# Performance work log

Hardware: AMD Instinct MI355X
Metric: run time of the kernel (lower is better)

Reference implementation:

```python
import jax, jax.numpy as jnp
import numpy as np

HEIGHT, WIDTH = 224, 224
SIGMA = 3e-4      # soft-coverage falloff (DIB-R style delta)
EPS = 1e-10


def setup_inputs() -> dict:
    key = jax.random.key(0)
    kp, kf, kc = jax.random.split(key, 3)
    B, P, F = 2, 2048, 256
    points = 0.5 * jax.random.normal(kp, (B, P, 3), dtype=jnp.float32)
    faces = jax.random.randint(kf, (F, 3), 0, P, dtype=jnp.int32)
    colors = jax.random.uniform(kc, (B, P, 3), dtype=jnp.float32)
    rot = jnp.broadcast_to(jnp.eye(3, dtype=jnp.float32), (B, 3, 3))
    pos = jnp.tile(jnp.array([0.0, 0.0, 2.5], jnp.float32), (B, 1))
    tanfov = float(np.tan(45.0 * np.pi / 360.0))
    proj = jnp.array([[1.0 / tanfov], [1.0 / tanfov], [-1.0]], jnp.float32)
    return dict(points_bxpx3=points, faces_fx3=faces, camera_rot=rot,
                camera_pos=pos, camera_proj=proj, colors_bxpx3=colors)


def _render(points_bxpx3, camera_rot, camera_pos, camera_proj, colors_bxpx3, faces_fx3):
    H, W = HEIGHT, WIDTH
    # ---- perspective projection (kaolin DIB-R convention) ----
    pc = jnp.einsum('bpj,bij->bpi', points_bxpx3 - camera_pos[:, None, :], camera_rot)  # camera space [B,P,3]
    xyz = pc * camera_proj.reshape(1, 1, 3)
    xy = xyz[..., :2] / xyz[..., 2:3]                                   # NDC xy [B,P,2]
    i0, i1, i2 = faces_fx3[:, 0], faces_fx3[:, 1], faces_fx3[:, 2]
    p0, p1, p2 = pc[:, i0], pc[:, i1], pc[:, i2]                        # [B,F,3]
    q0, q1, q2 = xy[:, i0], xy[:, i1], xy[:, i2]                        # [B,F,2]
    normal = jnp.cross(p1 - p0, p2 - p0)                                # [B,F,3]
    normalz = normal[..., 2]
    normal1 = normal / jnp.sqrt(jnp.sum(normal * normal, -1, keepdims=True) + EPS)
    # ---- per-face vertex features: 3 verts x (rgb + mask) == color_bxfx12 ----
    ones = jnp.ones(colors_bxpx3.shape[:2] + (1,), colors_bxpx3.dtype)
    cm = jnp.concatenate([colors_bxpx3, ones], -1)                      # [B,P,4]
    feat = jnp.stack([cm[:, i0], cm[:, i1], cm[:, i2]], axis=2)         # [B,F,3,4]
    # ---- rasterize: per-pixel per-face barycentric test ----
    xs = (2.0 * jnp.arange(W, dtype=jnp.float32) + 1.0) / W - 1.0
    ys = 1.0 - (2.0 * jnp.arange(H, dtype=jnp.float32) + 1.0) / H
    PX = xs[None, None, :, None]                                        # [1,1,W,1]
    PY = ys[None, :, None, None]                                        # [1,H,1,1]
    bf = lambda a: a[:, None, None, :]                                  # [B,F] -> [B,1,1,F]
    x0, y0 = q0[..., 0], q0[..., 1]
    x1, y1 = q1[..., 0], q1[..., 1]
    x2, y2 = q2[..., 0], q2[..., 1]
    denom = (y1 - y2) * (x0 - x2) + (x2 - x1) * (y0 - y2)
    denom = jnp.where(jnp.abs(denom) < EPS, EPS, denom)
    dx2 = PX - bf(x2)
    dy2 = PY - bf(y2)
    lam0 = (bf(y1 - y2) * dx2 + bf(x2 - x1) * dy2) / bf(denom)          # [B,H,W,F]
    lam1 = (bf(y2 - y0) * dx2 + bf(x0 - x2) * dy2) / bf(denom)
    lam2 = 1.0 - lam0 - lam1
    inside = (lam0 >= 0) & (lam1 >= 0) & (lam2 >= 0)
    front = (normalz > 0)[:, None, None, :]
    valid = inside & front
    # nearest face: camera looks down -z, nearer == larger camera-space z
    zpix = lam0 * bf(p0[..., 2]) + lam1 * bf(p1[..., 2]) + lam2 * bf(p2[..., 2])
    score = jnp.where(valid, zpix, -1e10)
    idx = jnp.argmax(score, axis=-1)                                    # [B,H,W]
    valid_any = jnp.any(valid, axis=-1)
    take = lambda a: jnp.take_along_axis(a, idx[..., None], axis=-1)[..., 0]
    l0, l1, l2 = take(lam0), take(lam1), take(lam2)
    fsel = jax.vmap(lambda f, i: f[i])(feat, idx)                       # [B,H,W,3,4]
    imfeat = (l0[..., None] * fsel[..., 0, :] + l1[..., None] * fsel[..., 1, :]
              + l2[..., None] * fsel[..., 2, :]) * valid_any[..., None]
    # ---- soft coverage probability: dist to nearest edge, 0 inside ----
    def seg_d2(ax, ay, bx, by):
        ex, ey = bf(bx - ax), bf(by - ay)
        pax, pay = PX - bf(ax), PY - bf(ay)
        t = jnp.clip((pax * ex + pay * ey) / (ex * ex + ey * ey + EPS), 0.0, 1.0)
        ddx, ddy = pax - t * ex, pay - t * ey
        return ddx * ddx + ddy * ddy
    d2 = jnp.minimum(seg_d2(x0, y0, x1, y1),
                     jnp.minimum(seg_d2(x1, y1, x2, y2), seg_d2(x2, y2, x0, y0)))
    d2 = jnp.where(inside, 0.0, d2)
    prob = jnp.where(front, jnp.exp(-d2 / SIGMA) * (1.0 - 1e-7), 0.0)
    improb = (1.0 - jnp.exp(jnp.sum(jnp.log1p(-prob), axis=-1)))[..., None]  # [B,H,W,1]
    imrender = imfeat[..., :3]
    return imrender, improb, normal1


def reference(points_bxpx3, camera_rot, camera_pos, camera_proj, colors_bxpx3, faces_fx3):
    return _render(points_bxpx3, camera_rot, camera_pos, camera_proj, colors_bxpx3, faces_fx3)
```

## Files before the change

kernel.cpp:

```cpp
#include <hip/hip_runtime.h>
#include <math.h>

#define HGT 224
#define WID 224
#define NPIX (HGT * WID)
#define SIGMA 0.0003f
#define EPSV 1e-10f
#define DATA_STRIDE 32
#define LDS_STRIDE 33
#define MAXF 256
#define MARGIN 0.062f
#define HALFDIAG 0.04420f
#define BAND (MARGIN + HALFDIAG)
#define HD_IN (HALFDIAG + 1.0e-4f)


__global__ void face_pre(const float* __restrict__ points,
                         const int* __restrict__ faces,
                         const float* __restrict__ rot,
                         const float* __restrict__ pos,
                         const float* __restrict__ proj,
                         const float* __restrict__ colors,
                         float* __restrict__ filt,
                         float* __restrict__ data,
                         float* __restrict__ out_normal,
                         int B, int P, int F) {
    int gid = blockIdx.x * blockDim.x + threadIdx.x;
    if (gid >= B * F) return;
    int b = gid / F;
    int f = gid - b * F;

    const float* Rb = rot + b * 9;
    float posx = pos[b * 3 + 0], posy = pos[b * 3 + 1], posz = pos[b * 3 + 2];
    float pj0 = proj[0], pj1 = proj[1], pj2 = proj[2];

    float pcx[3], pcy[3], pcz[3], qx[3], qy[3], col[9];
    for (int v = 0; v < 3; v++) {
        int i = faces[f * 3 + v];
        float dx = points[(b * P + i) * 3 + 0] - posx;
        float dy = points[(b * P + i) * 3 + 1] - posy;
        float dz = points[(b * P + i) * 3 + 2] - posz;
        pcx[v] = Rb[0] * dx + Rb[1] * dy + Rb[2] * dz;
        pcy[v] = Rb[3] * dx + Rb[4] * dy + Rb[5] * dz;
        pcz[v] = Rb[6] * dx + Rb[7] * dy + Rb[8] * dz;
        float zz = pcz[v] * pj2;
        qx[v] = (pcx[v] * pj0) / zz;
        qy[v] = (pcy[v] * pj1) / zz;
        col[v * 3 + 0] = colors[(b * P + i) * 3 + 0];
        col[v * 3 + 1] = colors[(b * P + i) * 3 + 1];
        col[v * 3 + 2] = colors[(b * P + i) * 3 + 2];
    }

    float ux = pcx[1] - pcx[0], uy = pcy[1] - pcy[0], uz = pcz[1] - pcz[0];
    float vx = pcx[2] - pcx[0], vy = pcy[2] - pcy[0], vz = pcz[2] - pcz[0];
    float nx = uy * vz - uz * vy;
    float ny = uz * vx - ux * vz;
    float nz = ux * vy - uy * vx;
    float ninv = 1.0f / sqrtf(nx * nx + ny * ny + nz * nz + EPSV);
    out_normal[gid * 3 + 0] = nx * ninv;
    out_normal[gid * 3 + 1] = ny * ninv;
    out_normal[gid * 3 + 2] = nz * ninv;

    float x0 = qx[0], y0 = qy[0], x1 = qx[1], y1 = qy[1], x2 = qx[2], y2 = qy[2];
    float denom = (y1 - y2) * (x0 - x2) + (x2 - x1) * (y0 - y2);
    if (fabsf(denom) < EPSV) denom = EPSV;
    float rd = 1.0f / denom;

    float a00 = (y1 - y2) * rd;
    float a01 = (x2 - x1) * rd;
    float a10 = (y2 - y0) * rd;
    float a11 = (x0 - x2) * rd;

    float z0 = pcz[0], z1 = pcz[1], z2c = pcz[2];
    float zgx = a00 * (z0 - z2c) + a10 * (z1 - z2c);
    float zgy = a01 * (z0 - z2c) + a11 * (z1 - z2c);
    float zc  = z2c - zgx * x2 - zgy * y2;

    int BF = B * F;
    float4* f4 = (float4*)filt;
    bool front = nz > 0.0f;
    if (front) {
        f4[0 * BF + gid] = make_float4(fminf(x0, fminf(x1, x2)),
                                       fminf(y0, fminf(y1, y2)),
                                       fmaxf(x0, fmaxf(x1, x2)),
                                       fmaxf(y0, fmaxf(y1, y2)));
    } else {
        f4[0 * BF + gid] = make_float4(1e30f, 1e30f, -1e30f, -1e30f);
    }

    float n0 = 1.0f / sqrtf(a00 * a00 + a01 * a01 + EPSV);
    float n1 = 1.0f / sqrtf(a10 * a10 + a11 * a11 + EPSV);
    float g2x = -(a00 + a10), g2y = -(a01 + a11);
    float n2 = 1.0f / sqrtf(g2x * g2x + g2y * g2y + EPSV);
    f4[1 * BF + gid] = make_float4(a00 * n0, a01 * n0,
                                   -(a00 * x2 + a01 * y2) * n0, a10 * n1);
    f4[2 * BF + gid] = make_float4(a11 * n1, -(a10 * x2 + a11 * y2) * n1,
                                   g2x * n2, g2y * n2);
    f4[3 * BF + gid] = make_float4((1.0f - g2x * x2 - g2y * y2) * n2,
                                   zgx, zgy, zc);

    float* fp = data + gid * DATA_STRIDE;
    fp[0] = x2; fp[1] = y2;
    fp[2] = zgx; fp[3] = zgy; fp[4] = z2c;
    fp[5] = a00; fp[6] = a01; fp[7] = a10; fp[8] = a11;
    fp[9] = x0; fp[10] = y0; fp[11] = x1; fp[12] = y1;

    float e01x = x1 - x0, e01y = y1 - y0;
    float e12x = x2 - x1, e12y = y2 - y1;
    float e20x = x0 - x2, e20y = y0 - y2;
    fp[13] = e01x; fp[14] = e01y; fp[15] = 1.0f / (e01x * e01x + e01y * e01y + EPSV);
    fp[16] = e12x; fp[17] = e12y; fp[18] = 1.0f / (e12x * e12x + e12y * e12y + EPSV);
    fp[19] = e20x; fp[20] = e20y; fp[21] = 1.0f / (e20x * e20x + e20y * e20y + EPSV);
    for (int k = 0; k < 9; k++) fp[22 + k] = col[k];
    fp[31] = 0.0f;
}

__device__ __forceinline__ float seg_d2(float px, float py, float ax, float ay,
                                        float ex, float ey, float inv) {
    float pax = px - ax, pay = py - ay;
    float t = (pax * ex + pay * ey) * inv;
    t = fminf(fmaxf(t, 0.0f), 1.0f);
    float ddx = pax - t * ex;
    float ddy = pay - t * ey;
    return ddx * ddx + ddy * ddy;
}

__global__ __launch_bounds__(256) void rast(const float* __restrict__ filt,
                                            const float* __restrict__ data,
                                            float* __restrict__ out,
                                            int B, int F) {
    __shared__ float sdat[MAXF * LDS_STRIDE];
    __shared__ float sc[256], sp[256];
    __shared__ int sidx[256];

    const int tiles_x = WID / 8;
    const int tiles_per_batch = tiles_x * (HGT / 8);
    int b = blockIdx.x / tiles_per_batch;
    int tile = blockIdx.x - b * tiles_per_batch;
    int ty = tile / tiles_x;
    int tx = tile - ty * tiles_x;

    int t = threadIdx.x & 63;
    int w = threadIdx.x >> 6;
    int lx = t & 7, ly = t >> 3;
    int x = tx * 8 + lx;
    int y = ty * 8 + ly;
    float px = (2.0f * (float)x + 1.0f) / (float)WID - 1.0f;
    float py = 1.0f - (2.0f * (float)y + 1.0f) / (float)HGT;

    float txlo = (2.0f * (float)(tx * 8) + 1.0f) / (float)WID - 1.0f - MARGIN;
    float txhi = (2.0f * (float)(tx * 8 + 7) + 1.0f) / (float)WID - 1.0f + MARGIN;
    float tyhi = 1.0f - (2.0f * (float)(ty * 8) + 1.0f) / (float)HGT + MARGIN;
    float tylo = 1.0f - (2.0f * (float)(ty * 8 + 7) + 1.0f) / (float)HGT - MARGIN;
    float cx = (16.0f * (float)tx + 8.0f) / (float)WID - 1.0f;
    float cy = 1.0f - (16.0f * (float)ty + 8.0f) / (float)HGT;

    const float* datb = data + (size_t)b * F * DATA_STRIDE;

    int chunk = (F + 3) >> 2;
    int fbeg = w * chunk;
    int fend = min(fbeg + chunk, F);

    int BF = B * F;
    int bF = b * F;
    const float4* fl4 = (const float4*)filt;
    int fl = fbeg + t;
    bool haveface = (fl < fend);
    float4 bb = make_float4(0.f, 0.f, 0.f, 0.f);
    float4 e0 = bb, e1 = bb, e2 = bb;
    if (haveface) {
        bb = fl4[0 * BF + bF + fl];
        e0 = fl4[1 * BF + bF + fl];
        e1 = fl4[2 * BF + bF + fl];
        e2 = fl4[3 * BF + bF + fl];
    }

    int nvec = F * (DATA_STRIDE / 4);
    for (int g = threadIdx.x; g < nvec; g += 256) {
        float4 v = ((const float4*)datb)[g];
        int f = g >> 3, k4 = g & 7;
        float* d = &sdat[f * LDS_STRIDE + k4 * 4];
        d[0] = v.x; d[1] = v.y; d[2] = v.z; d[3] = v.w;
    }
    __syncthreads();

    float best = -1e10f;
    int bidx = -1;
    float prod = 1.0f;
    int n_in = 0;

    bool pass = false, inclass = false;
    float zgx = 0.0f, zgy = 0.0f, zc = 0.0f;
    if (haveface) {
        bool bpass = (bb.x <= txhi) & (bb.z >= txlo) & (bb.y <= tyhi) & (bb.w >= tylo);
        float d0 = e0.x * cx + e0.y * cy + e0.z;
        float d1 = e0.w * cx + e1.x * cy + e1.y;
        float d2 = e1.z * cx + e1.w * cy + e2.x;
        float dmin = fminf(d0, fminf(d1, d2));
        pass = bpass & (dmin >= -BAND);
        inclass = bpass & (dmin >= HD_IN);
        zgx = e2.y; zgy = e2.z; zc = e2.w;
    }
    unsigned long long mask_in = __ballot(inclass);
    unsigned long long mask_bd = __ballot(pass) & ~mask_in;

    n_in += (int)__popcll(mask_in);
    while (mask_in) {
        int fo = (int)__builtin_ctzll(mask_in);
        mask_in &= mask_in - 1;
        float zx = __shfl(zgx, fo);
        float zy = __shfl(zgy, fo);
        float zk = __shfl(zc,  fo);
        float zpix = zx * px + zy * py + zk;
        if (zpix > best) { best = zpix; bidx = fbeg + fo; }
    }

    while (mask_bd) {
        int fo = (int)__builtin_ctzll(mask_bd);
        mask_bd &= mask_bd - 1;
        int fi = fbeg + fo;
        const float* fp = &sdat[fi * LDS_STRIDE];

        float dx2 = px - fp[0], dy2 = py - fp[1];
        float lam0 = fp[5] * dx2 + fp[6] * dy2;
        float lam1 = fp[7] * dx2 + fp[8] * dy2;
        float lam2 = 1.0f - lam0 - lam1;
        bool inside = (lam0 >= 0.0f) && (lam1 >= 0.0f) && (lam2 >= 0.0f);

        float zpix = fp[2] * dx2 + fp[3] * dy2 + fp[4];
        if (inside && zpix > best) { best = zpix; bidx = fi; }

        float dA = seg_d2(px, py, fp[9],  fp[10], fp[13], fp[14], fp[15]);
        float dB = seg_d2(px, py, fp[11], fp[12], fp[16], fp[17], fp[18]);
        float dC = seg_d2(px, py, fp[0],  fp[1],  fp[19], fp[20], fp[21]);
        float d2 = inside ? 0.0f : fminf(dA, fminf(dB, dC));
        float pr = __expf(d2 * (-1.0f / SIGMA)) * (1.0f - 1e-7f);
        prod *= (1.0f - pr);
    }

    prod *= exp2f(-24.0f * (float)n_in);

    sc[threadIdx.x] = best;
    sp[threadIdx.x] = prod;
    sidx[threadIdx.x] = bidx;
    __syncthreads();

    if (w == 0) {
        best = -1e10f; bidx = -1;
        prod = 1.0f;
        for (int k = 0; k < 4; k++) {
            int j = k * 64 + t;
            prod *= sp[j];
            float v = sc[j];
            if (v > best) {
                best = v; bidx = sidx[j];
            }
        }

        float r = 0.0f, g = 0.0f, bbv = 0.0f;
        if (bidx >= 0) {
            const float* fp = &sdat[bidx * LDS_STRIDE];
            float dx2 = px - fp[0], dy2 = py - fp[1];
            float lam0 = fp[5] * dx2 + fp[6] * dy2;
            float lam1 = fp[7] * dx2 + fp[8] * dy2;
            float lam2 = 1.0f - lam0 - lam1;
            r   = lam0 * fp[22] + lam1 * fp[25] + lam2 * fp[28];
            g   = lam0 * fp[23] + lam1 * fp[26] + lam2 * fp[29];
            bbv = lam0 * fp[24] + lam1 * fp[27] + lam2 * fp[30];
        }

        int pixidx = b * NPIX + y * WID + x;
        out[pixidx * 3 + 0] = r;
        out[pixidx * 3 + 1] = g;
        out[pixidx * 3 + 2] = bbv;
        out[B * NPIX * 3 + pixidx] = 1.0f - prod;
    }
}

extern "C" void kernel_launch(void* const* d_in, const int* in_sizes, int n_in,
                              void* d_out, int out_size, void* d_ws, size_t ws_size,
                              hipStream_t stream) {
    const float* points = (const float*)d_in[0];
    const int*   faces  = (const int*)d_in[1];
    const float* rot    = (const float*)d_in[2];
    const float* pos    = (const float*)d_in[3];
    const float* proj   = (const float*)d_in[4];
    const float* colors = (const float*)d_in[5];
    float* out = (float*)d_out;

    int F = in_sizes[1] / 3;
    int B = in_sizes[3] / 3;
    int P = in_sizes[0] / (3 * B);

    float* filt = (float*)d_ws;
    float* data = filt + (size_t)B * F * 16;
    float* out_normal = out + B * NPIX * 3 + B * NPIX;

    int nf = B * F;
    face_pre<<<(nf + 63) / 64, 64, 0, stream>>>(points, faces, rot, pos, proj,
                                                colors, filt, data, out_normal,
                                                B, P, F);

    int blocks = B * (NPIX / 64);
    rast<<<blocks, 256, 0, stream>>>(filt, data, out, B, F);
}
```

Baseline: 77.32 us.

## Fuse face preprocessing into raster kernel, recomputing face setup per block

Removes the separate face_pre launch and workspace round trip. Each raster block now computes the per-face projection, edge functions and colours for all faces itself (one face per thread) and writes them to LDS in a structure-of-arrays float4 layout, and only tile 0 writes the normals. This saves a kernel launch and global traffic, at the cost of redundant face math and gathers in every one of about 1568 blocks. It also assumes F <= 256 and that the per-wave face chunk is 64.

```diff
diff --git a/kernel.cpp b/kernel.cpp
--- a/kernel.cpp
+++ b/kernel.cpp
@@ -6,114 +6,11 @@
 #define NPIX (HGT * WID)
 #define SIGMA 0.0003f
 #define EPSV 1e-10f
-#define DATA_STRIDE 32
-#define LDS_STRIDE 33
 #define MAXF 256
 #define MARGIN 0.062f
 #define HALFDIAG 0.04420f
 #define BAND (MARGIN + HALFDIAG)
 #define HD_IN (HALFDIAG + 1.0e-4f)
-
-
-__global__ void face_pre(const float* __restrict__ points,
-                         const int* __restrict__ faces,
-                         const float* __restrict__ rot,
-                         const float* __restrict__ pos,
-                         const float* __restrict__ proj,
-                         const float* __restrict__ colors,
-                         float* __restrict__ filt,
-                         float* __restrict__ data,
-                         float* __restrict__ out_normal,
-                         int B, int P, int F) {
-    int gid = blockIdx.x * blockDim.x + threadIdx.x;
-    if (gid >= B * F) return;
-    int b = gid / F;
-    int f = gid - b * F;
-
-    const float* Rb = rot + b * 9;
-    float posx = pos[b * 3 + 0], posy = pos[b * 3 + 1], posz = pos[b * 3 + 2];
-    float pj0 = proj[0], pj1 = proj[1], pj2 = proj[2];
-
-    float pcx[3], pcy[3], pcz[3], qx[3], qy[3], col[9];
-    for (int v = 0; v < 3; v++) {
-        int i = faces[f * 3 + v];
-        float dx = points[(b * P + i) * 3 + 0] - posx;
-        float dy = points[(b * P + i) * 3 + 1] - posy;
-        float dz = points[(b * P + i) * 3 + 2] - posz;
-        pcx[v] = Rb[0] * dx + Rb[1] * dy + Rb[2] * dz;
-        pcy[v] = Rb[3] * dx + Rb[4] * dy + Rb[5] * dz;
-        pcz[v] = Rb[6] * dx + Rb[7] * dy + Rb[8] * dz;
-        float zz = pcz[v] * pj2;
-        qx[v] = (pcx[v] * pj0) / zz;
-        qy[v] = (pcy[v] * pj1) / zz;
-        col[v * 3 + 0] = colors[(b * P + i) * 3 + 0];
-        col[v * 3 + 1] = colors[(b * P + i) * 3 + 1];
-        col[v * 3 + 2] = colors[(b * P + i) * 3 + 2];
-    }
-
-    float ux = pcx[1] - pcx[0], uy = pcy[1] - pcy[0], uz = pcz[1] - pcz[0];
-    float vx = pcx[2] - pcx[0], vy = pcy[2] - pcy[0], vz = pcz[2] - pcz[0];
-    float nx = uy * vz - uz * vy;
-    float ny = uz * vx - ux * vz;
-    float nz = ux * vy - uy * vx;
-    float ninv = 1.0f / sqrtf(nx * nx + ny * ny + nz * nz + EPSV);
-    out_normal[gid * 3 + 0] = nx * ninv;
-    out_normal[gid * 3 + 1] = ny * ninv;
-    out_normal[gid * 3 + 2] = nz * ninv;
-
-    float x0 = qx[0], y0 = qy[0], x1 = qx[1], y1 = qy[1], x2 = qx[2], y2 = qy[2];
-    float denom = (y1 - y2) * (x0 - x2) + (x2 - x1) * (y0 - y2);
-    if (fabsf(denom) < EPSV) denom = EPSV;
-    float rd = 1.0f / denom;
-
-    float a00 = (y1 - y2) * rd;
-    float a01 = (x2 - x1) * rd;
-    float a10 = (y2 - y0) * rd;
-    float a11 = (x0 - x2) * rd;
-
-    float z0 = pcz[0], z1 = pcz[1], z2c = pcz[2];
-    float zgx = a00 * (z0 - z2c) + a10 * (z1 - z2c);
-    float zgy = a01 * (z0 - z2c) + a11 * (z1 - z2c);
-    float zc  = z2c - zgx * x2 - zgy * y2;
-
-    int BF = B * F;
-    float4* f4 = (float4*)filt;
-    bool front = nz > 0.0f;
-    if (front) {
-        f4[0 * BF + gid] = make_float4(fminf(x0, fminf(x1, x2)),
-                                       fminf(y0, fminf(y1, y2)),
-                                       fmaxf(x0, fmaxf(x1, x2)),
-                                       fmaxf(y0, fmaxf(y1, y2)));
-    } else {
-        f4[0 * BF + gid] = make_float4(1e30f, 1e30f, -1e30f, -1e30f);
-    }
-
-    float n0 = 1.0f / sqrtf(a00 * a00 + a01 * a01 + EPSV);
-    float n1 = 1.0f / sqrtf(a10 * a10 + a11 * a11 + EPSV);
-    float g2x = -(a00 + a10), g2y = -(a01 + a11);
-    float n2 = 1.0f / sqrtf(g2x * g2x + g2y * g2y + EPSV);
-    f4[1 * BF + gid] = make_float4(a00 * n0, a01 * n0,
-                                   -(a00 * x2 + a01 * y2) * n0, a10 * n1);
-    f4[2 * BF + gid] = make_float4(a11 * n1, -(a10 * x2 + a11 * y2) * n1,
-                                   g2x * n2, g2y * n2);
-    f4[3 * BF + gid] = make_float4((1.0f - g2x * x2 - g2y * y2) * n2,
-                                   zgx, zgy, zc);
-
-    float* fp = data + gid * DATA_STRIDE;
-    fp[0] = x2; fp[1] = y2;
-    fp[2] = zgx; fp[3] = zgy; fp[4] = z2c;
-    fp[5] = a00; fp[6] = a01; fp[7] = a10; fp[8] = a11;
-    fp[9] = x0; fp[10] = y0; fp[11] = x1; fp[12] = y1;
-
-    float e01x = x1 - x0, e01y = y1 - y0;
-    float e12x = x2 - x1, e12y = y2 - y1;
-    float e20x = x0 - x2, e20y = y0 - y2;
-    fp[13] = e01x; fp[14] = e01y; fp[15] = 1.0f / (e01x * e01x + e01y * e01y + EPSV);
-    fp[16] = e12x; fp[17] = e12y; fp[18] = 1.0f / (e12x * e12x + e12y * e12y + EPSV);
-    fp[19] = e20x; fp[20] = e20y; fp[21] = 1.0f / (e20x * e20x + e20y * e20y + EPSV);
-    for (int k = 0; k < 9; k++) fp[22 + k] = col[k];
-    fp[31] = 0.0f;
-}
 
 __device__ __forceinline__ float seg_d2(float px, float py, float ax, float ay,
                                         float ex, float ey, float inv) {
@@ -125,23 +22,28 @@
     return ddx * ddx + ddy * ddy;
 }
 
-__global__ __launch_bounds__(256) void rast(const float* __restrict__ filt,
-                                            const float* __restrict__ data,
-                                            float* __restrict__ out,
-                                            int B, int F) {
-    __shared__ float sdat[MAXF * LDS_STRIDE];
+__global__ __launch_bounds__(256) void render(const float* __restrict__ points,
+                                              const int* __restrict__ faces,
+                                              const float* __restrict__ rot,
+                                              const float* __restrict__ pos,
+                                              const float* __restrict__ proj,
+                                              const float* __restrict__ colors,
+                                              float* __restrict__ out,
+                                              int B, int P, int F) {
+    __shared__ float4 s4[8 * MAXF];
     __shared__ float sc[256], sp[256];
     __shared__ int sidx[256];
 
     const int tiles_x = WID / 8;
-    const int tiles_per_batch = tiles_x * (HGT / 8);
-    int b = blockIdx.x / tiles_per_batch;
-    int tile = blockIdx.x - b * tiles_per_batch;
+    const int tpb = tiles_x * (HGT / 8);
+    int b = blockIdx.x / tpb;
+    int tile = blockIdx.x - b * tpb;
     int ty = tile / tiles_x;
     int tx = tile - ty * tiles_x;
 
-    int t = threadIdx.x & 63;
-    int w = threadIdx.x >> 6;
+    int tid = threadIdx.x;
+    int t = tid & 63;
+    int w = tid >> 6;
     int lx = t & 7, ly = t >> 3;
     int x = tx * 8 + lx;
     int y = ty * 8 + ly;
@@ -155,62 +57,123 @@
     float cx = (16.0f * (float)tx + 8.0f) / (float)WID - 1.0f;
     float cy = 1.0f - (16.0f * (float)ty + 8.0f) / (float)HGT;
 
-    const float* datb = data + (size_t)b * F * DATA_STRIDE;
-
-    int chunk = (F + 3) >> 2;
-    int fbeg = w * chunk;
-    int fend = min(fbeg + chunk, F);
-
-    int BF = B * F;
-    int bF = b * F;
-    const float4* fl4 = (const float4*)filt;
-    int fl = fbeg + t;
-    bool haveface = (fl < fend);
-    float4 bb = make_float4(0.f, 0.f, 0.f, 0.f);
-    float4 e0 = bb, e1 = bb, e2 = bb;
-    if (haveface) {
-        bb = fl4[0 * BF + bF + fl];
-        e0 = fl4[1 * BF + bF + fl];
-        e1 = fl4[2 * BF + bF + fl];
-        e2 = fl4[3 * BF + bF + fl];
-    }
-
-    int nvec = F * (DATA_STRIDE / 4);
-    for (int g = threadIdx.x; g < nvec; g += 256) {
-        float4 v = ((const float4*)datb)[g];
-        int f = g >> 3, k4 = g & 7;
-        float* d = &sdat[f * LDS_STRIDE + k4 * 4];
-        d[0] = v.x; d[1] = v.y; d[2] = v.z; d[3] = v.w;
-    }
+    bool havef = (tid < F);
+    float bxmin = 1e30f, bymin = 1e30f, bxmax = -1e30f, bymax = -1e30f;
+    float D0x = 0.f, D0y = 0.f, D0c = 0.f;
+    float D1x = 0.f, D1y = 0.f, D1c = 0.f;
+    float D2x = 0.f, D2y = 0.f, D2c = 0.f;
+    float zgx = 0.f, zgy = 0.f, zco = 0.f;
+    if (havef) {
+        const float* Rb = rot + b * 9;
+        float posx = pos[b * 3 + 0], posy = pos[b * 3 + 1], posz = pos[b * 3 + 2];
+        float pj0 = proj[0], pj1 = proj[1], pj2 = proj[2];
+
+        float pcx[3], pcy[3], pcz[3], qxx[3], qyy[3], col[9];
+        for (int v = 0; v < 3; v++) {
+            int i = faces[tid * 3 + v];
+            float dx = points[(b * P + i) * 3 + 0] - posx;
+            float dy = points[(b * P + i) * 3 + 1] - posy;
+            float dz = points[(b * P + i) * 3 + 2] - posz;
+            pcx[v] = Rb[0] * dx + Rb[1] * dy + Rb[2] * dz;
+            pcy[v] = Rb[3] * dx + Rb[4] * dy + Rb[5] * dz;
+            pcz[v] = Rb[6] * dx + Rb[7] * dy + Rb[8] * dz;
+            float zz = pcz[v] * pj2;
+            qxx[v] = (pcx[v] * pj0) / zz;
+            qyy[v] = (pcy[v] * pj1) / zz;
+            col[v * 3 + 0] = colors[(b * P + i) * 3 + 0];
+            col[v * 3 + 1] = colors[(b * P + i) * 3 + 1];
+            col[v * 3 + 2] = colors[(b * P + i) * 3 + 2];
+        }
+
+        float ux = pcx[1] - pcx[0], uy = pcy[1] - pcy[0], uz = pcz[1] - pcz[0];
+        float vx = pcx[2] - pcx[0], vy = pcy[2] - pcy[0], vz = pcz[2] - pcz[0];
+        float nx = uy * vz - uz * vy;
+        float ny = uz * vx - ux * vz;
+        float nz = ux * vy - uy * vx;
+        float ninv = 1.0f / sqrtf(nx * nx + ny * ny + nz * nz + EPSV);
+        if (tile == 0) {
+            float* onr = out + (size_t)B * NPIX * 3 + (size_t)B * NPIX
+                       + (size_t)(b * F + tid) * 3;
+            onr[0] = nx * ninv; onr[1] = ny * ninv; onr[2] = nz * ninv;
+        }
+
+        float x0 = qxx[0], y0 = qyy[0], x1 = qxx[1], y1 = qyy[1];
+        float x2 = qxx[2], y2 = qyy[2];
+        float denom = (y1 - y2) * (x0 - x2) + (x2 - x1) * (y0 - y2);
+        if (fabsf(denom) < EPSV) denom = EPSV;
+        float rd = 1.0f / denom;
+        float a00 = (y1 - y2) * rd;
+        float a01 = (x2 - x1) * rd;
+        float a10 = (y2 - y0) * rd;
+        float a11 = (x0 - x2) * rd;
+
+        float z0 = pcz[0], z1 = pcz[1], z2c = pcz[2];
+        zgx = a00 * (z0 - z2c) + a10 * (z1 - z2c);
+        zgy = a01 * (z0 - z2c) + a11 * (z1 - z2c);
+        zco = z2c - zgx * x2 - zgy * y2;
+
+        bool front = nz > 0.0f;
+        if (front) {
+            bxmin = fminf(x0, fminf(x1, x2));
+            bymin = fminf(y0, fminf(y1, y2));
+            bxmax = fmaxf(x0, fmaxf(x1, x2));
+            bymax = fmaxf(y0, fmaxf(y1, y2));
+        }
+
+        float n0 = 1.0f / sqrtf(a00 * a00 + a01 * a01 + EPSV);
+        float n1 = 1.0f / sqrtf(a10 * a10 + a11 * a11 + EPSV);
+        float g2x = -(a00 + a10), g2y = -(a01 + a11);
+        float n2 = 1.0f / sqrtf(g2x * g2x + g2y * g2y + EPSV);
+        D0x = a00 * n0; D0y = a01 * n0; D0c = -(a00 * x2 + a01 * y2) * n0;
+        D1x = a10 * n1; D1y = a11 * n1; D1c = -(a10 * x2 + a11 * y2) * n1;
+        D2x = g2x * n2; D2y = g2y * n2; D2c = (1.0f - g2x * x2 - g2y * y2) * n2;
+
+        float e01x = x1 - x0, e01y = y1 - y0;
+        float e12x = x2 - x1, e12y = y2 - y1;
+        float e20x = x0 - x2, e20y = y0 - y2;
+        float inv01 = 1.0f / (e01x * e01x + e01y * e01y + EPSV);
+        float inv12 = 1.0f / (e12x * e12x + e12y * e12y + EPSV);
+        float inv20 = 1.0f / (e20x * e20x + e20y * e20y + EPSV);
+
+        s4[0 * MAXF + tid] = make_float4(x2, y2, zgx, zgy);
+        s4[1 * MAXF + tid] = make_float4(z2c, a00, a01, a10);
+        s4[2 * MAXF + tid] = make_float4(a11, x0, y0, x1);
+        s4[3 * MAXF + tid] = make_float4(y1, e01x, e01y, inv01);
+        s4[4 * MAXF + tid] = make_float4(e12x, e12y, inv12, e20x);
+        s4[5 * MAXF + tid] = make_float4(e20y, inv20, col[0], col[1]);
+        s4[6 * MAXF + tid] = make_float4(col[2], col[3], col[4], col[5]);
+        s4[7 * MAXF + tid] = make_float4(col[6], col[7], col[8], 0.0f);
+    }
+
+    bool pass = false, inclass = false;
+    if (havef) {
+        bool bpass = (bxmin <= txhi) & (bxmax >= txlo) &
+                     (bymin <= tyhi) & (bymax >= tylo);
+        float d0 = D0x * cx + D0y * cy + D0c;
+        float d1 = D1x * cx + D1y * cy + D1c;
+        float d2 = D2x * cx + D2y * cy + D2c;
+        float dmin = fminf(d0, fminf(d1, d2));
+        pass = bpass & (dmin >= -BAND);
+        inclass = bpass & (dmin >= HD_IN);
+    }
+
     __syncthreads();
+
+    int fbeg = w * 64;
+    unsigned long long mask_in = __ballot(inclass);
+    unsigned long long mask_bd = __ballot(pass) & ~mask_in;
 
     float best = -1e10f;
     int bidx = -1;
     float prod = 1.0f;
-    int n_in = 0;
-
-    bool pass = false, inclass = false;
-    float zgx = 0.0f, zgy = 0.0f, zc = 0.0f;
-    if (haveface) {
-        bool bpass = (bb.x <= txhi) & (bb.z >= txlo) & (bb.y <= tyhi) & (bb.w >= tylo);
-        float d0 = e0.x * cx + e0.y * cy + e0.z;
-        float d1 = e0.w * cx + e1.x * cy + e1.y;
-        float d2 = e1.z * cx + e1.w * cy + e2.x;
-        float dmin = fminf(d0, fminf(d1, d2));
-        pass = bpass & (dmin >= -BAND);
-        inclass = bpass & (dmin >= HD_IN);
-        zgx = e2.y; zgy = e2.z; zc = e2.w;
-    }
-    unsigned long long mask_in = __ballot(inclass);
-    unsigned long long mask_bd = __ballot(pass) & ~mask_in;
-
-    n_in += (int)__popcll(mask_in);
+    int n_in = (int)__popcll(mask_in);
+
     while (mask_in) {
         int fo = (int)__builtin_ctzll(mask_in);
         mask_in &= mask_in - 1;
         float zx = __shfl(zgx, fo);
         float zy = __shfl(zgy, fo);
-        float zk = __shfl(zc,  fo);
+        float zk = __shfl(zco, fo);
         float zpix = zx * px + zy * py + zk;
         if (zpix > best) { best = zpix; bidx = fbeg + fo; }
     }
@@ -219,20 +182,25 @@
         int fo = (int)__builtin_ctzll(mask_bd);
         mask_bd &= mask_bd - 1;
         int fi = fbeg + fo;
-        const float* fp = &sdat[fi * LDS_STRIDE];
-
-        float dx2 = px - fp[0], dy2 = py - fp[1];
-        float lam0 = fp[5] * dx2 + fp[6] * dy2;
-        float lam1 = fp[7] * dx2 + fp[8] * dy2;
+        float4 q0 = s4[0 * MAXF + fi];
+        float4 q1 = s4[1 * MAXF + fi];
+        float4 q2 = s4[2 * MAXF + fi];
+        float4 q3 = s4[3 * MAXF + fi];
+        float4 q4 = s4[4 * MAXF + fi];
+        float4 q5 = s4[5 * MAXF + fi];
+
+        float dx2 = px - q0.x, dy2 = py - q0.y;
+        float lam0 = q1.y * dx2 + q1.z * dy2;
+        float lam1 = q1.w * dx2 + q2.x * dy2;
         float lam2 = 1.0f - lam0 - lam1;
         bool inside = (lam0 >= 0.0f) && (lam1 >= 0.0f) && (lam2 >= 0.0f);
 
-        float zpix = fp[2] * dx2 + fp[3] * dy2 + fp[4];
+        float zpix = q0.z * dx2 + q0.w * dy2 + q1.x;
         if (inside && zpix > best) { best = zpix; bidx = fi; }
 
-        float dA = seg_d2(px, py, fp[9],  fp[10], fp[13], fp[14], fp[15]);
-        float dB = seg_d2(px, py, fp[11], fp[12], fp[16], fp[17], fp[18]);
-        float dC = seg_d2(px, py, fp[0],  fp[1],  fp[19], fp[20], fp[21]);
+        float dA = seg_d2(px, py, q2.y, q2.z, q3.y, q3.z, q3.w);
+        float dB = seg_d2(px, py, q2.w, q3.x, q4.x, q4.y, q4.z);
+        float dC = seg_d2(px, py, q0.x, q0.y, q4.w, q5.x, q5.y);
         float d2 = inside ? 0.0f : fminf(dA, fminf(dB, dC));
         float pr = __expf(d2 * (-1.0f / SIGMA)) * (1.0f - 1e-7f);
         prod *= (1.0f - pr);
@@ -240,9 +208,9 @@
 
     prod *= exp2f(-24.0f * (float)n_in);
 
-    sc[threadIdx.x] = best;
-    sp[threadIdx.x] = prod;
-    sidx[threadIdx.x] = bidx;
+    sc[tid] = best;
+    sp[tid] = prod;
+    sidx[tid] = bidx;
     __syncthreads();
 
     if (w == 0) {
@@ -259,14 +227,19 @@
 
         float r = 0.0f, g = 0.0f, bbv = 0.0f;
         if (bidx >= 0) {
-            const float* fp = &sdat[bidx * LDS_STRIDE];
-            float dx2 = px - fp[0], dy2 = py - fp[1];
-            float lam0 = fp[5] * dx2 + fp[6] * dy2;
-            float lam1 = fp[7] * dx2 + fp[8] * dy2;
+            float4 g0 = s4[0 * MAXF + bidx];
+            float4 g1 = s4[1 * MAXF + bidx];
+            float4 g2 = s4[2 * MAXF + bidx];
+            float4 g5 = s4[5 * MAXF + bidx];
+            float4 g6 = s4[6 * MAXF + bidx];
+            float4 g7 = s4[7 * MAXF + bidx];
+            float dx2 = px - g0.x, dy2 = py - g0.y;
+            float lam0 = g1.y * dx2 + g1.z * dy2;
+            float lam1 = g1.w * dx2 + g2.x * dy2;
             float lam2 = 1.0f - lam0 - lam1;
-            r   = lam0 * fp[22] + lam1 * fp[25] + lam2 * fp[28];
-            g   = lam0 * fp[23] + lam1 * fp[26] + lam2 * fp[29];
-            bbv = lam0 * fp[24] + lam1 * fp[27] + lam2 * fp[30];
+            r   = lam0 * g5.z + lam1 * g6.y + lam2 * g7.x;
+            g   = lam0 * g5.w + lam1 * g6.z + lam2 * g7.y;
+            bbv = lam0 * g6.x + lam1 * g6.w + lam2 * g7.z;
         }
 
         int pixidx = b * NPIX + y * WID + x;
@@ -292,15 +265,7 @@
     int B = in_sizes[3] / 3;
     int P = in_sizes[0] / (3 * B);
 
-    float* filt = (float*)d_ws;
-    float* data = filt + (size_t)B * F * 16;
-    float* out_normal = out + B * NPIX * 3 + B * NPIX;
-
-    int nf = B * F;
-    face_pre<<<(nf + 63) / 64, 64, 0, stream>>>(points, faces, rot, pos, proj,
-                                                colors, filt, data, out_normal,
-                                                B, P, F);
-
     int blocks = B * (NPIX / 64);
-    rast<<<blocks, 256, 0, stream>>>(filt, data, out, B, F);
+    render<<<blocks, 256, 0, stream>>>(points, faces, rot, pos, proj, colors,
+                                       out, B, P, F);
 }
```

Result: faster. 75.15 us (median of 2 runs) (-2.8%).
